# Kernel optimization log

Hardware: AMD Instinct MI355X
Metric: run time of the kernel (lower is better)

The kernel has to match this reference:

```python
import jax, jax.numpy as jnp
import numpy as np

ATT_H = 256
DEC_H = 512
CTX = 1024  # 2 * encoder_hidden_size


def setup_inputs() -> dict:
    key = jax.random.key(0)
    ks = jax.random.split(key, 8)
    B, T = 32, 4096
    prev = jax.random.normal(ks[0], (B, 1, DEC_H), dtype=jnp.float32)
    enc = jax.random.normal(ks[1], (B, T, CTX), dtype=jnp.float32)
    # nn.Linear params: weight [out,in], bias [out]
    W_w = jax.random.normal(ks[2], (ATT_H, DEC_H), dtype=jnp.float32) / np.sqrt(DEC_H)
    W_b = jax.random.normal(ks[3], (ATT_H,), dtype=jnp.float32) * 0.01
    U_w = jax.random.normal(ks[4], (ATT_H, CTX), dtype=jnp.float32) / np.sqrt(CTX)
    U_b = jax.random.normal(ks[5], (ATT_H,), dtype=jnp.float32) * 0.01
    v = jax.random.uniform(ks[6], (ATT_H,), dtype=jnp.float32)
    return {
        "batch_size": B,
        "max_seq_len": T,
        "previous_decoder_hidden_state": prev,
        "encoder_final_hidden_layers": enc,
        "W_w": W_w, "W_b": W_b, "U_w": U_w, "U_b": U_b, "v": v,
    }


def reference(batch_size, max_seq_len, previous_decoder_hidden_state,
              encoder_final_hidden_layers, W_w, W_b, U_w, U_b, v):
    # tmp_1: [B,1,H] = W(prev); tmp_3: [B,T,H] = U(enc)
    tmp1 = jnp.einsum('bod,hd->boh', previous_decoder_hidden_state, W_w) + W_b
    tmp3 = jnp.einsum('btc,hc->bth', encoder_final_hidden_layers, U_w) + U_b
    # energy: [B,T] = relu(tmp1 + tmp3) . v
    energy = jnp.einsum('bth,h->bt', jax.nn.relu(tmp1 + tmp3), v)
    alpha = jax.nn.softmax(energy, axis=1)  # [B,T]
    # weighted sum over time -> context [B, 2E]
    c = jnp.einsum('bt,btc->bc', alpha, encoder_final_hidden_layers)
    return c
```

## Files before the change

kernel.cpp:

```cpp
#include <hip/hip_runtime.h>
#include <hip/hip_bf16.h>

#define BB   32
#define TT   4096
#define CTXD 1024
#define HH   256
#define DH   512
#define BT   64
#define NTILES (TT/BT)
#define BK   32
#define NKT  (CTXD/BK)
#define LDA  1032
#define LDU  40
#define SMEM_BYTES (BT*LDA*2 + HH*LDU*2 + 4*BT*4 + BT*4)

typedef __attribute__((ext_vector_type(8))) short bf16x8;
typedef __attribute__((ext_vector_type(4))) float f32x4;

static __device__ __forceinline__ unsigned short f2bf(float f) {
    unsigned int u = __float_as_uint(f);
    u += 0x7FFF + ((u >> 16) & 1);
    return (unsigned short)(u >> 16);
}
static __device__ __forceinline__ unsigned pack2(float x, float y) {
    return (unsigned)f2bf(x) | ((unsigned)f2bf(y) << 16);
}
static __device__ __forceinline__ float bf2f(unsigned short u) {
    return __uint_as_float((unsigned)u << 16);
}

__global__ void uconv_kernel(const float* __restrict__ Uw, unsigned short* __restrict__ Ub) {
    int idx = blockIdx.x * blockDim.x + threadIdx.x;
    float4 u4 = ((const float4*)Uw)[idx];
    ushort4 o;
    o.x = f2bf(u4.x); o.y = f2bf(u4.y); o.z = f2bf(u4.z); o.w = f2bf(u4.w);
    ((ushort4*)Ub)[idx] = o;
}

__global__ void bias_kernel(const float* __restrict__ prev, const float* __restrict__ Ww,
                            const float* __restrict__ Wb, const float* __restrict__ Ubias,
                            float* __restrict__ bias) {
    __shared__ float ps[DH];
    int b = blockIdx.x, h = threadIdx.x;
    if (h < DH / 4) ((float4*)ps)[h] = ((const float4*)(prev + (size_t)b * DH))[h];
    __syncthreads();
    float acc = Wb[h] + Ubias[h];
    const float4* wr = (const float4*)(Ww + (size_t)h * DH);
    #pragma unroll 4
    for (int d = 0; d < DH / 4; ++d) {
        float4 w4 = wr[d];
        float4 p4 = ((const float4*)ps)[d];
        acc += w4.x * p4.x + w4.y * p4.y + w4.z * p4.z + w4.w * p4.w;
    }
    bias[b * HH + h] = acc;
}

__global__ __launch_bounds__(256, 1)
void attn_main(const float* __restrict__ enc, const unsigned short* __restrict__ Ub,
               const float* __restrict__ bias, const float* __restrict__ v,
               float* __restrict__ partO, float* __restrict__ partM,
               float* __restrict__ partL) {
    extern __shared__ __align__(16) char smem[];
    unsigned short* As = (unsigned short*)smem;
    unsigned short* Us = (unsigned short*)(smem + BT * LDA * 2);
    float* epart = (float*)(smem + BT * LDA * 2 + HH * LDU * 2);
    float* pbuf  = epart + 4 * BT;

    const int tid  = threadIdx.x;
    const int lane = tid & 63;
    const int w    = tid >> 6;
    const int quad = lane >> 4;
    const int l15  = lane & 15;
    const int b    = blockIdx.x & 31;
    const int tile = blockIdx.x >> 5;
    const int t0   = tile * BT;
    const int pi   = b * NTILES + tile;

    const int srow = tid >> 2;
    const int sg   = tid & 3;
    const float*          gA = enc + ((size_t)b * TT + t0 + srow) * CTXD + sg * 8;
    const unsigned short* gU = Ub + (size_t)srow * CTXD + sg * 8;

    f32x4 acc[4][4];
    #pragma unroll
    for (int mi = 0; mi < 4; ++mi)
        #pragma unroll
        for (int ni = 0; ni < 4; ++ni) acc[mi][ni] = (f32x4){0.f, 0.f, 0.f, 0.f};

    float4 ca0 = *(const float4*)(gA);
    float4 ca1 = *(const float4*)(gA + 4);
    uint4  cu0 = *(const uint4*)(gU);
    uint4  cu1 = *(const uint4*)(gU + (size_t)64 * CTXD);
    uint4  cu2 = *(const uint4*)(gU + (size_t)128 * CTXD);
    uint4  cu3 = *(const uint4*)(gU + (size_t)192 * CTXD);

    for (int kt = 0; kt < NKT; ++kt) {
        int ktn = (kt + 1 < NKT) ? kt + 1 : kt;
        float4 na0 = *(const float4*)(gA + ktn * BK);
        float4 na1 = *(const float4*)(gA + ktn * BK + 4);
        uint4  nu0 = *(const uint4*)(gU + ktn * BK);
        uint4  nu1 = *(const uint4*)(gU + (size_t)64 * CTXD + ktn * BK);
        uint4  nu2 = *(const uint4*)(gU + (size_t)128 * CTXD + ktn * BK);
        uint4  nu3 = *(const uint4*)(gU + (size_t)192 * CTXD + ktn * BK);

        __syncthreads();
        uint4 pa;
        pa.x = pack2(ca0.x, ca0.y); pa.y = pack2(ca0.z, ca0.w);
        pa.z = pack2(ca1.x, ca1.y); pa.w = pack2(ca1.z, ca1.w);
        *(uint4*)&As[srow * LDA + kt * BK + sg * 8] = pa;
        *(uint4*)&Us[(srow      ) * LDU + sg * 8] = cu0;
        *(uint4*)&Us[(srow +  64) * LDU + sg * 8] = cu1;
        *(uint4*)&Us[(srow + 128) * LDU + sg * 8] = cu2;
        *(uint4*)&Us[(srow + 192) * LDU + sg * 8] = cu3;
        __syncthreads();

        bf16x8 af[4], bfr[4];
        #pragma unroll
        for (int mi = 0; mi < 4; ++mi)
            af[mi] = *(const bf16x8*)&As[(mi * 16 + l15) * LDA + kt * BK + quad * 8];
        #pragma unroll
        for (int ni = 0; ni < 4; ++ni)
            bfr[ni] = *(const bf16x8*)&Us[(w * 64 + ni * 16 + l15) * LDU + quad * 8];
        #pragma unroll
        for (int mi = 0; mi < 4; ++mi)
            #pragma unroll
            for (int ni = 0; ni < 4; ++ni)
                acc[mi][ni] = __builtin_amdgcn_mfma_f32_16x16x32_bf16(af[mi], bfr[ni], acc[mi][ni], 0, 0, 0);

        ca0 = na0; ca1 = na1; cu0 = nu0; cu1 = nu1; cu2 = nu2; cu3 = nu3;
    }

    float vv[4], bb[4];
    #pragma unroll
    for (int ni = 0; ni < 4; ++ni) {
        int h = w * 64 + ni * 16 + l15;
        vv[ni] = v[h];
        bb[ni] = bias[b * HH + h];
    }
    #pragma unroll
    for (int mi = 0; mi < 4; ++mi) {
        #pragma unroll
        for (int r = 0; r < 4; ++r) {
            float e = 0.f;
            #pragma unroll
            for (int ni = 0; ni < 4; ++ni) {
                float x = acc[mi][ni][r] + bb[ni];
                e += fmaxf(x, 0.f) * vv[ni];
            }
            e += __shfl_xor(e, 1);
            e += __shfl_xor(e, 2);
            e += __shfl_xor(e, 4);
            e += __shfl_xor(e, 8);
            if (l15 == 0) epart[w * BT + mi * 16 + quad * 4 + r] = e;
        }
    }
    __syncthreads();

    if (tid < 64) {
        float e = epart[0 * BT + tid] + epart[1 * BT + tid] + epart[2 * BT + tid] + epart[3 * BT + tid];
        float m = e;
        #pragma unroll
        for (int off = 32; off; off >>= 1) m = fmaxf(m, __shfl_xor(m, off));
        float p = __expf(e - m);
        float l = p;
        #pragma unroll
        for (int off = 32; off; off >>= 1) l += __shfl_xor(l, off);
        pbuf[tid] = p;
        if (tid == 0) { partM[pi] = m; partL[pi] = l; }
    }
    __syncthreads();

    const int c4 = tid * 4;
    float o0 = 0.f, o1 = 0.f, o2 = 0.f, o3 = 0.f;
    #pragma unroll 8
    for (int t = 0; t < BT; ++t) {
        float p = pbuf[t];
        ushort4 e4 = *(const ushort4*)&As[t * LDA + c4];
        o0 += p * bf2f(e4.x);
        o1 += p * bf2f(e4.y);
        o2 += p * bf2f(e4.z);
        o3 += p * bf2f(e4.w);
    }
    float4 r4; r4.x = o0; r4.y = o1; r4.z = o2; r4.w = o3;
    *(float4*)(partO + (size_t)pi * CTXD + c4) = r4;
}

__global__ void combine_kernel(const float* __restrict__ partO, const float* __restrict__ partM,
                               const float* __restrict__ partL, float* __restrict__ out) {
    __shared__ float sc[NTILES];
    __shared__ float sL;
    int b = blockIdx.x, tid = threadIdx.x;
    if (tid < 64) {
        float m = partM[b * NTILES + tid];
        float l = partL[b * NTILES + tid];
        float M = m;
        #pragma unroll
        for (int off = 32; off; off >>= 1) M = fmaxf(M, __shfl_xor(M, off));
        float s = __expf(m - M);
        sc[tid] = s;
        float Lp = l * s;
        #pragma unroll
        for (int off = 32; off; off >>= 1) Lp += __shfl_xor(Lp, off);
        if (tid == 0) sL = Lp;
    }
    __syncthreads();
    float4 o = {0.f, 0.f, 0.f, 0.f};
    const float* base = partO + (size_t)b * NTILES * CTXD;
    #pragma unroll 4
    for (int i = 0; i < NTILES; ++i) {
        float s = sc[i];
        float4 p4 = *(const float4*)(base + (size_t)i * CTXD + tid * 4);
        o.x += s * p4.x; o.y += s * p4.y; o.z += s * p4.z; o.w += s * p4.w;
    }
    float inv = 1.0f / sL;
    float4 r; r.x = o.x * inv; r.y = o.y * inv; r.z = o.z * inv; r.w = o.w * inv;
    ((float4*)out)[b * (CTXD / 4) + tid] = r;
}

extern "C" void kernel_launch(void* const* d_in, const int* in_sizes, int n_in,
                              void* d_out, int out_size, void* d_ws, size_t ws_size,
                              hipStream_t stream) {
    const float* prev  = (const float*)d_in[2];
    const float* enc   = (const float*)d_in[3];
    const float* Ww    = (const float*)d_in[4];
    const float* Wb    = (const float*)d_in[5];
    const float* Uw    = (const float*)d_in[6];
    const float* Ubias = (const float*)d_in[7];
    const float* v     = (const float*)d_in[8];
    float* out = (float*)d_out;

    char* ws = (char*)d_ws;
    float* bias          = (float*)ws;
    unsigned short* Ub   = (unsigned short*)(ws + 32768);
    float* partO         = (float*)(ws + 32768 + 524288);
    float* partM         = partO + (size_t)BB * NTILES * CTXD;
    float* partL         = partM + BB * NTILES;

    static int lds_set = 0;
    hipFuncSetAttribute((const void*)attn_main,
                        hipFuncAttributeMaxDynamicSharedMemorySize, SMEM_BYTES);
    (void)lds_set;

    uconv_kernel<<<dim3(256), dim3(256), 0, stream>>>(Uw, Ub);
    bias_kernel<<<dim3(BB), dim3(HH), 0, stream>>>(prev, Ww, Wb, Ubias, bias);
    attn_main<<<dim3(BB * NTILES), dim3(256), SMEM_BYTES, stream>>>(enc, Ub, bias, v, partO, partM, partL);
    combine_kernel<<<dim3(BB), dim3(256), 0, stream>>>(partO, partM, partL, out);
}
```

Baseline: 864.9 us.

## Load U fragments directly to registers and deepen encoder prefetch pipeline

Removes the LDS staging of the bf16 U weight tile: each wave now loads its MFMA B fragments straight from global memory (L2-resident) into registers, with one-step prefetch. The encoder A tile gets a three-deep register prefetch, and the next k-slice is written to LDS while the current one is consumed, so one barrier per iteration replaces two. The aim is to cut LDS traffic and synchronisation and hide global load latency, at the cost of more registers and uncoalesced per-lane global loads of U.

```diff
diff --git a/kernel.cpp b/kernel.cpp
--- a/kernel.cpp
+++ b/kernel.cpp
@@ -11,8 +11,7 @@
 #define BK   32
 #define NKT  (CTXD/BK)
 #define LDA  1032
-#define LDU  40
-#define SMEM_BYTES (BT*LDA*2 + HH*LDU*2 + 4*BT*4 + BT*4)
+#define SMEM_BYTES (BT*LDA*2 + 4*BT*4 + BT*4)
 
 typedef __attribute__((ext_vector_type(8))) short bf16x8;
 typedef __attribute__((ext_vector_type(4))) float f32x4;
@@ -62,8 +61,7 @@
                float* __restrict__ partL) {
     extern __shared__ __align__(16) char smem[];
     unsigned short* As = (unsigned short*)smem;
-    unsigned short* Us = (unsigned short*)(smem + BT * LDA * 2);
-    float* epart = (float*)(smem + BT * LDA * 2 + HH * LDU * 2);
+    float* epart = (float*)(smem + BT * LDA * 2);
     float* pbuf  = epart + 4 * BT;
 
     const int tid  = threadIdx.x;
@@ -78,8 +76,12 @@
 
     const int srow = tid >> 2;
     const int sg   = tid & 3;
-    const float*          gA = enc + ((size_t)b * TT + t0 + srow) * CTXD + sg * 8;
-    const unsigned short* gU = Ub + (size_t)srow * CTXD + sg * 8;
+    const float* gA = enc + ((size_t)b * TT + t0 + srow) * CTXD + sg * 8;
+
+    const unsigned short* gB0 = Ub + (size_t)(w * 64 +  0 + l15) * CTXD + quad * 8;
+    const unsigned short* gB1 = Ub + (size_t)(w * 64 + 16 + l15) * CTXD + quad * 8;
+    const unsigned short* gB2 = Ub + (size_t)(w * 64 + 32 + l15) * CTXD + quad * 8;
+    const unsigned short* gB3 = Ub + (size_t)(w * 64 + 48 + l15) * CTXD + quad * 8;
 
     f32x4 acc[4][4];
     #pragma unroll
@@ -87,47 +89,56 @@
         #pragma unroll
         for (int ni = 0; ni < 4; ++ni) acc[mi][ni] = (f32x4){0.f, 0.f, 0.f, 0.f};
 
-    float4 ca0 = *(const float4*)(gA);
-    float4 ca1 = *(const float4*)(gA + 4);
-    uint4  cu0 = *(const uint4*)(gU);
-    uint4  cu1 = *(const uint4*)(gU + (size_t)64 * CTXD);
-    uint4  cu2 = *(const uint4*)(gU + (size_t)128 * CTXD);
-    uint4  cu3 = *(const uint4*)(gU + (size_t)192 * CTXD);
+    float4 c0a = *(const float4*)(gA);
+    float4 c0b = *(const float4*)(gA + 4);
+    float4 p0a = *(const float4*)(gA + BK);
+    float4 p0b = *(const float4*)(gA + BK + 4);
+    float4 p1a = *(const float4*)(gA + 2 * BK);
+    float4 p1b = *(const float4*)(gA + 2 * BK + 4);
+    bf16x8 bcur0 = *(const bf16x8*)(gB0);
+    bf16x8 bcur1 = *(const bf16x8*)(gB1);
+    bf16x8 bcur2 = *(const bf16x8*)(gB2);
+    bf16x8 bcur3 = *(const bf16x8*)(gB3);
+    {
+        uint4 pa;
+        pa.x = pack2(c0a.x, c0a.y); pa.y = pack2(c0a.z, c0a.w);
+        pa.z = pack2(c0b.x, c0b.y); pa.w = pack2(c0b.z, c0b.w);
+        *(uint4*)&As[srow * LDA + sg * 8] = pa;
+    }
+    __syncthreads();
 
     for (int kt = 0; kt < NKT; ++kt) {
-        int ktn = (kt + 1 < NKT) ? kt + 1 : kt;
-        float4 na0 = *(const float4*)(gA + ktn * BK);
-        float4 na1 = *(const float4*)(gA + ktn * BK + 4);
-        uint4  nu0 = *(const uint4*)(gU + ktn * BK);
-        uint4  nu1 = *(const uint4*)(gU + (size_t)64 * CTXD + ktn * BK);
-        uint4  nu2 = *(const uint4*)(gU + (size_t)128 * CTXD + ktn * BK);
-        uint4  nu3 = *(const uint4*)(gU + (size_t)192 * CTXD + ktn * BK);
-
-        __syncthreads();
-        uint4 pa;
-        pa.x = pack2(ca0.x, ca0.y); pa.y = pack2(ca0.z, ca0.w);
-        pa.z = pack2(ca1.x, ca1.y); pa.w = pack2(ca1.z, ca1.w);
-        *(uint4*)&As[srow * LDA + kt * BK + sg * 8] = pa;
-        *(uint4*)&Us[(srow      ) * LDU + sg * 8] = cu0;
-        *(uint4*)&Us[(srow +  64) * LDU + sg * 8] = cu1;
-        *(uint4*)&Us[(srow + 128) * LDU + sg * 8] = cu2;
-        *(uint4*)&Us[(srow + 192) * LDU + sg * 8] = cu3;
-        __syncthreads();
-
-        bf16x8 af[4], bfr[4];
+        int ln = kt + 3 < NKT ? kt + 3 : NKT - 1;
+        float4 n0 = *(const float4*)(gA + ln * BK);
+        float4 n1 = *(const float4*)(gA + ln * BK + 4);
+        int bn = kt + 1 < NKT ? kt + 1 : NKT - 1;
+        bf16x8 bn0 = *(const bf16x8*)(gB0 + bn * BK);
+        bf16x8 bn1 = *(const bf16x8*)(gB1 + bn * BK);
+        bf16x8 bn2 = *(const bf16x8*)(gB2 + bn * BK);
+        bf16x8 bn3 = *(const bf16x8*)(gB3 + bn * BK);
+
+        if (kt + 1 < NKT) {
+            uint4 pa;
+            pa.x = pack2(p0a.x, p0a.y); pa.y = pack2(p0a.z, p0a.w);
+            pa.z = pack2(p0b.x, p0b.y); pa.w = pack2(p0b.z, p0b.w);
+            *(uint4*)&As[srow * LDA + (kt + 1) * BK + sg * 8] = pa;
+        }
+
+        bf16x8 af[4];
         #pragma unroll
         for (int mi = 0; mi < 4; ++mi)
             af[mi] = *(const bf16x8*)&As[(mi * 16 + l15) * LDA + kt * BK + quad * 8];
         #pragma unroll
-        for (int ni = 0; ni < 4; ++ni)
-            bfr[ni] = *(const bf16x8*)&Us[(w * 64 + ni * 16 + l15) * LDU + quad * 8];
-        #pragma unroll
-        for (int mi = 0; mi < 4; ++mi)
-            #pragma unroll
-            for (int ni = 0; ni < 4; ++ni)
-                acc[mi][ni] = __builtin_amdgcn_mfma_f32_16x16x32_bf16(af[mi], bfr[ni], acc[mi][ni], 0, 0, 0);
-
-        ca0 = na0; ca1 = na1; cu0 = nu0; cu1 = nu1; cu2 = nu2; cu3 = nu3;
+        for (int mi = 0; mi < 4; ++mi) {
+            acc[mi][0] = __builtin_amdgcn_mfma_f32_16x16x32_bf16(af[mi], bcur0, acc[mi][0], 0, 0, 0);
+            acc[mi][1] = __builtin_amdgcn_mfma_f32_16x16x32_bf16(af[mi], bcur1, acc[mi][1], 0, 0, 0);
+            acc[mi][2] = __builtin_amdgcn_mfma_f32_16x16x32_bf16(af[mi], bcur2, acc[mi][2], 0, 0, 0);
+            acc[mi][3] = __builtin_amdgcn_mfma_f32_16x16x32_bf16(af[mi], bcur3, acc[mi][3], 0, 0, 0);
+        }
+        __syncthreads();
+
+        p0a = p1a; p0b = p1b; p1a = n0; p1b = n1;
+        bcur0 = bn0; bcur1 = bn1; bcur2 = bn2; bcur3 = bn3;
     }
 
     float vv[4], bb[4];
@@ -236,10 +247,8 @@
     float* partM         = partO + (size_t)BB * NTILES * CTXD;
     float* partL         = partM + BB * NTILES;
 
-    static int lds_set = 0;
     hipFuncSetAttribute((const void*)attn_main,
                         hipFuncAttributeMaxDynamicSharedMemorySize, SMEM_BYTES);
-    (void)lds_set;
 
     uconv_kernel<<<dim3(256), dim3(256), 0, stream>>>(Uw, Ub);
     bias_kernel<<<dim3(BB), dim3(HH), 0, stream>>>(prev, Ww, Wb, Ubias, bias);
```

Result: slower. 889.1 us (+2.8%).
